# Performance work log

Measured on AMD Instinct MI355X. Metric: run time of the kernel, lower is better.

The kernel has to match this reference:

```python
import jax, jax.numpy as jnp
import numpy as np

B, S, D, NH, DH = 2, 1024, 1024, 16, 64
BLOCK_SIZES = [4, 4, 4]
SCALE = 1.0 / (DH ** 0.5)
INF = 1000000.0
LN_EPS = 1e-9


def _pos_embeds(seq_len, d_model):
    # Funnel 'factorized' sinusoidal relative position embeddings (phi, pi, psi, omega)
    pos = jnp.arange(seq_len, dtype=jnp.float32)
    freq = jnp.arange(d_model // 2, dtype=jnp.float32)
    inv_freq = 1.0 / (10000.0 ** (freq / (d_model // 2)))
    sinusoid = pos[:, None] * inv_freq[None]
    s, c = jnp.sin(sinusoid), jnp.cos(sinusoid)
    phi = jnp.concatenate([s, s], axis=-1)
    psi = jnp.concatenate([c, s], axis=-1)
    pi = jnp.concatenate([c, c], axis=-1)
    omega = jnp.concatenate([-s, c], axis=-1)
    return phi, pi, psi, omega


def _layer_norm(x, g, b):
    mu = jnp.mean(x, axis=-1, keepdims=True)
    var = jnp.mean((x - mu) ** 2, axis=-1, keepdims=True)
    return (x - mu) * jax.lax.rsqrt(var + LN_EPS) * g + b


def _attn_layer(q_in, kv, phi_q, pi_q, psi_k, om_k, tt_mat, mask, W):
    # FunnelRelMultiheadAttentionDecoder.forward (dropout=0, eval)
    (wq, bq, wk, bk, wv, bv, rw, rr, rs, rk, seg, wp, bp, g, b) = W
    Bq, Lq, _ = q_in.shape
    Lk = kv.shape[1]
    q = (q_in @ wq + bq).reshape(Bq, Lq, NH, DH) * SCALE
    k = (kv @ wk + bk).reshape(Bq, Lk, NH, DH)
    v = (kv @ wv + bv).reshape(Bq, Lk, NH, DH)
    content = jnp.einsum('bind,bjnd->bnij', q + rw * SCALE, k)
    # factorized relative positional attention
    q_r = jnp.einsum('binh,dnh->bind', q + rr * SCALE, rk)  # [B,Lq,NH,D]
    pos = (jnp.einsum('bind,jd->bnij', q_r * phi_q[:, None], psi_k)
           + jnp.einsum('bind,jd->bnij', q_r * pi_q[:, None], om_k))
    # relative token-type attention
    ttb = jnp.einsum('bind,snd->bnis', q + rs * SCALE, seg)  # [B,NH,Lq,2]
    tok = jnp.where(tt_mat[:, None], ttb[..., 1:2], ttb[..., 0:1])
    score = (content + pos + tok).astype(jnp.float32)
    score = score - INF * (1.0 - mask[:, None, :, None].astype(jnp.float32))
    prob = jax.nn.softmax(score, axis=-1).astype(q_in.dtype)
    vec = jnp.einsum('bnij,bjnd->bind', prob, v).reshape(Bq, Lq, NH * DH)
    return _layer_norm(q_in + vec @ wp + bp, g, b)


def _upsample(h, target):
    # _upsample_hidden: interleave hidden with avg of (hidden, roll(hidden, 1))
    shifted = jnp.roll(h, 1, axis=1)
    interp = 0.5 * (h + shifted)
    out = jnp.stack([h, interp], axis=2).reshape(h.shape[0], -1, h.shape[2])
    if out.shape[1] > target:
        out = out[:, :-1]
    return out


def _forward(final_hidden, block_h0, block_h1, block_h2, attention_mask, token_type_ids,
             Wq, bq, Wk, bk, Wv, bv, r_w_bias, r_r_bias, r_s_bias, r_kernel, seg_embed,
             Wpost, bpost, ln_g, ln_b):
    block_hs = [block_h0, block_h1, block_h2]
    # init_attention_inputs
    ids = token_type_ids
    cls_ids = ids == 2
    tt = (ids[:, :, None] == ids[:, None]) | (cls_ids[:, :, None] | cls_ids[:, None])
    phi, pi, psi, omega = _pos_embeds(S, D)
    mask = attention_mask
    # replay encoder-side pooling schedule (pool_q_only, separate_cls=False)
    inputs = {}
    for bi, bs in enumerate(BLOCK_SIZES):
        pooling = bi > 0
        if pooling:
            phi, pi = phi[::2], pi[::2]          # pre_attention_pooling
            tt = tt[:, ::2, :]
        for li in range(bs):
            inputs[(bi, li)] = (phi, pi, psi, omega, tt, mask)
            if li == 0 and pooling:              # post_attention_pooling
                psi, omega = psi[::2], omega[::2]
                tt = tt[:, :, ::2]
                mask = jnp.min(mask.reshape(mask.shape[0], -1, 2), axis=-1)
    # decoder pass (skip_w == 0 so skip mixing is identity)
    offsets = np.cumsum([0] + BLOCK_SIZES)
    hidden = final_hidden
    for bi in reversed(range(len(BLOCK_SIZES))):
        upflag = hidden.shape[1] < block_hs[0].shape[1] and bi > 0
        if upflag:
            up = _upsample(hidden, block_hs[bi - 1].shape[1])
        for li in reversed(range(BLOCK_SIZES[bi])):
            l = int(offsets[bi]) + li
            phi_, pi_, psi_, om_, tt_, m_ = inputs[(bi, li)]
            do_up = upflag and li == 0
            if do_up:
                q_in, kv = up, hidden
                # query is the long (pre-pool) side: use context-length phi/pi on keys
                phi_q, pi_q, psi_k, om_k = psi_, om_, phi_, pi_
            else:
                q_in = kv = hidden
                phi_q, pi_q, psi_k, om_k = phi_, pi_, psi_, om_
            W = (Wq[l], bq[l], Wk[l], bk[l], Wv[l], bv[l], r_w_bias[l], r_r_bias[l],
                 r_s_bias[l], r_kernel[l], seg_embed[l], Wpost[l], bpost[l], ln_g[l], ln_b[l])
            hidden = _attn_layer(q_in, kv, phi_q, pi_q, psi_k, om_k,
                                 jnp.swapaxes(tt_, 1, 2), m_, W)
    return hidden


def setup_inputs() -> dict:
    key = jax.random.key(0)
    ks = jax.random.split(key, 20)
    L = sum(BLOCK_SIZES)
    w = lambda k, shape: jax.random.normal(k, shape, dtype=jnp.float32) * 0.02
    return {
        'final_hidden': jax.random.normal(ks[0], (B, S // 4, D), dtype=jnp.float32),
        'block_h0': jax.random.normal(ks[1], (B, S, D), dtype=jnp.float32),
        'block_h1': jax.random.normal(ks[2], (B, S // 2, D), dtype=jnp.float32),
        'block_h2': jax.random.normal(ks[3], (B, S // 4, D), dtype=jnp.float32),
        'attention_mask': jnp.ones((B, S), dtype=jnp.float32),
        'token_type_ids': jax.random.randint(ks[4], (B, S), 0, 2, dtype=jnp.int32),
        'Wq': w(ks[5], (L, D, D)), 'bq': jnp.zeros((L, D), jnp.float32),
        'Wk': w(ks[6], (L, D, D)), 'bk': jnp.zeros((L, D), jnp.float32),
        'Wv': w(ks[7], (L, D, D)), 'bv': jnp.zeros((L, D), jnp.float32),
        'r_w_bias': w(ks[8], (L, NH, DH)),
        'r_r_bias': w(ks[9], (L, NH, DH)),
        'r_s_bias': w(ks[10], (L, NH, DH)),
        'r_kernel': w(ks[11], (L, D, NH, DH)),
        'seg_embed': w(ks[12], (L, 2, NH, DH)),
        'Wpost': w(ks[13], (L, D, D)), 'bpost': jnp.zeros((L, D), jnp.float32),
        'ln_g': jnp.ones((L, D), jnp.float32), 'ln_b': jnp.zeros((L, D), jnp.float32),
    }


def reference(final_hidden, block_h0, block_h1, block_h2, attention_mask, token_type_ids,
              Wq, bq, Wk, bk, Wv, bv, r_w_bias, r_r_bias, r_s_bias, r_kernel, seg_embed,
              Wpost, bpost, ln_g, ln_b):
    return _forward(final_hidden, block_h0, block_h1, block_h2, attention_mask,
                    token_type_ids, Wq, bq, Wk, bk, Wv, bv, r_w_bias, r_r_bias,
                    r_s_bias, r_kernel, seg_embed, Wpost, bpost, ln_g, ln_b)
```

## Files before the change

kernel.cpp:

```cpp
#include <hip/hip_runtime.h>
#include <math.h>

#define NHEAD 16
#define DMODEL 1024
#define BATCH 2
#define QSCALE 0.125f

typedef __attribute__((ext_vector_type(8))) short bf16x8;
typedef __attribute__((ext_vector_type(4))) float f32x4;

__device__ inline unsigned short f2bf(float x) {
  unsigned int u = __float_as_uint(x);
  u += 0x7FFF + ((u >> 16) & 1);
  return (unsigned short)(u >> 16);
}
__device__ inline float bf2f(unsigned short h) {
  return __uint_as_float(((unsigned int)h) << 16);
}

typedef __attribute__((address_space(1))) const unsigned int gu32;
typedef __attribute__((address_space(3))) unsigned int lu32;
__device__ inline void gl_lds16(const unsigned short* g, unsigned short* l) {
  __builtin_amdgcn_global_load_lds((gu32*)g, (lu32*)l, 16, 0, 0);
}

template<int MODE>
__global__ __launch_bounds__(256) void gemm_bf16(
    const unsigned short* __restrict__ A, const unsigned short* __restrict__ Bt,
    const float* __restrict__ bias, const unsigned short* __restrict__ R,
    void* __restrict__ Cv, int M, int N, int K, int nrel)
{
  __shared__ __align__(16) unsigned short smem[32 * 512];
  const int tid = threadIdx.x;
  const int lane = tid & 63, w = tid >> 6;
  const int mw = w >> 1, nw = w & 1;
  const int bm = blockIdx.x * 128, bn = blockIdx.y * 128;
  const int lm = lane & 15, lq = lane >> 4;
  float* Cf = (float*)Cv;
  unsigned short* Cb = (unsigned short*)Cv;

  f32x4 acc[4][4];
#pragma unroll
  for (int i = 0; i < 4; ++i)
#pragma unroll
    for (int j = 0; j < 4; ++j) acc[i][j] = (f32x4){0.f, 0.f, 0.f, 0.f};

  for (int k0 = 0; k0 < K; k0 += 64) {
#pragma unroll
    for (int f = w; f < 16; f += 4) {
      const int kb = f >> 3, mb = f & 7;
      const int gr = bm + mb * 16 + lm;
      const int gc = k0 + kb * 32 + lq * 8;
      gl_lds16(A + (size_t)gr * K + gc, &smem[f * 512]);
      gl_lds16(Bt + (size_t)(bn + mb * 16 + lm) * K + gc, &smem[(16 + f) * 512]);
    }
    __syncthreads();
#pragma unroll
    for (int kb = 0; kb < 2; ++kb) {
      bf16x8 af[4], bf[4];
#pragma unroll
      for (int i = 0; i < 4; ++i)
        af[i] = *(const bf16x8*)(&smem[(kb * 8 + mw * 4 + i) * 512 + lane * 8]);
#pragma unroll
      for (int j = 0; j < 4; ++j)
        bf[j] = *(const bf16x8*)(&smem[(16 + kb * 8 + nw * 4 + j) * 512 + lane * 8]);
#pragma unroll
      for (int i = 0; i < 4; ++i)
#pragma unroll
        for (int j = 0; j < 4; ++j)
          acc[i][j] = __builtin_amdgcn_mfma_f32_16x16x32_bf16(
              af[i], bf[j], acc[i][j], 0, 0, 0);
    }
    __syncthreads();
  }
#pragma unroll
  for (int i = 0; i < 4; ++i) {
#pragma unroll
    for (int j = 0; j < 4; ++j) {
      const int col = bn + nw * 64 + j * 16 + lm;
      if (col >= N) continue;
#pragma unroll
      for (int r = 0; r < 4; ++r) {
        const int row = bm + mw * 64 + i * 16 + lq * 4 + r;
        float vv = acc[i][j][r];
        if (MODE == 1) vv = (vv + bias[col]) * QSCALE;
        else if (MODE == 2) vv = vv + bias[col] + bf2f(R[(size_t)row * N + col]);
        if (MODE == 3)
          Cb[(((size_t)(row >> 6)) * nrel + col) * 64 + (row & 63)] = f2bf(vv);
        else
          Cf[(size_t)row * N + col] = vv;
      }
    }
  }
}

__global__ __launch_bounds__(256) void gemm_qkv(
    const unsigned short* __restrict__ A, const unsigned short* __restrict__ Bt,
    const float* __restrict__ bq, const float* __restrict__ bk,
    const float* __restrict__ bv, float* __restrict__ Cq,
    unsigned short* __restrict__ Ck, unsigned short* __restrict__ Cv,
    int M, int K, int colbase)
{
  __shared__ __align__(16) unsigned short smem[32 * 512];
  const int tid = threadIdx.x;
  const int lane = tid & 63, w = tid >> 6;
  const int mw = w >> 1, nw = w & 1;
  const int bm = blockIdx.x * 128, bn = colbase + blockIdx.y * 128;
  const int lm = lane & 15, lq = lane >> 4;

  f32x4 acc[4][4];
#pragma unroll
  for (int i = 0; i < 4; ++i)
#pragma unroll
    for (int j = 0; j < 4; ++j) acc[i][j] = (f32x4){0.f, 0.f, 0.f, 0.f};

  for (int k0 = 0; k0 < K; k0 += 64) {
#pragma unroll
    for (int f = w; f < 16; f += 4) {
      const int kb = f >> 3, mb = f & 7;
      const int gr = bm + mb * 16 + lm;
      const int gc = k0 + kb * 32 + lq * 8;
      gl_lds16(A + (size_t)gr * K + gc, &smem[f * 512]);
      gl_lds16(Bt + (size_t)(bn + mb * 16 + lm) * K + gc, &smem[(16 + f) * 512]);
    }
    __syncthreads();
#pragma unroll
    for (int kb = 0; kb < 2; ++kb) {
      bf16x8 af[4], bf[4];
#pragma unroll
      for (int i = 0; i < 4; ++i)
        af[i] = *(const bf16x8*)(&smem[(kb * 8 + mw * 4 + i) * 512 + lane * 8]);
#pragma unroll
      for (int j = 0; j < 4; ++j)
        bf[j] = *(const bf16x8*)(&smem[(16 + kb * 8 + nw * 4 + j) * 512 + lane * 8]);
#pragma unroll
      for (int i = 0; i < 4; ++i)
#pragma unroll
        for (int j = 0; j < 4; ++j)
          acc[i][j] = __builtin_amdgcn_mfma_f32_16x16x32_bf16(
              af[i], bf[j], acc[i][j], 0, 0, 0);
    }
    __syncthreads();
  }
  const int which = bn >> 10;
  const float* bias = (which == 0) ? bq : (which == 1) ? bk : bv;
#pragma unroll
  for (int i = 0; i < 4; ++i) {
#pragma unroll
    for (int j = 0; j < 4; ++j) {
      const int col = bn + nw * 64 + j * 16 + lm;
      const int nc = col & 1023;
#pragma unroll
      for (int r = 0; r < 4; ++r) {
        const int row = bm + mw * 64 + i * 16 + lq * 4 + r;
        const float vv = acc[i][j][r] + bias[nc];
        if (which == 0)
          Cq[(size_t)row * 1024 + nc] = vv * QSCALE;
        else if (which == 1)
          Ck[(size_t)row * 1024 + nc] = f2bf(vv);
        else
          Cv[(size_t)row * 1024 + nc] = f2bf(vv);
      }
    }
  }
}

__global__ __launch_bounds__(256) void tpose5_k(
    const float* __restrict__ s0, const float* __restrict__ s1,
    const float* __restrict__ s2, const float* __restrict__ s3,
    const float* __restrict__ s4, unsigned short* __restrict__ d0,
    unsigned short* __restrict__ d1, unsigned short* __restrict__ d2,
    unsigned short* __restrict__ d3, unsigned short* __restrict__ d4)
{
  const float* in;
  unsigned short* out;
  switch (blockIdx.z) {
    case 0: in = s0; out = d0; break;
    case 1: in = s1; out = d1; break;
    case 2: in = s2; out = d2; break;
    case 3: in = s3; out = d3; break;
    default: in = s4; out = d4; break;
  }
  __shared__ float t[32][33];
  const int bi = blockIdx.x * 32, bj = blockIdx.y * 32;
  const int r = threadIdx.x >> 3, c4 = (threadIdx.x & 7) * 4;
  const float4 v = *(const float4*)(in + (size_t)(bi + r) * 1024 + bj + c4);
  t[r][c4] = v.x; t[r][c4 + 1] = v.y; t[r][c4 + 2] = v.z; t[r][c4 + 3] = v.w;
  __syncthreads();
  ushort4 o;
  o.x = f2bf(t[c4 + 0][r]); o.y = f2bf(t[c4 + 1][r]);
  o.z = f2bf(t[c4 + 2][r]); o.w = f2bf(t[c4 + 3][r]);
  *(ushort4*)(out + (size_t)(bj + r) * 1024 + bi + c4) = o;
}

__global__ void cvt_k(const float* __restrict__ in,
                      unsigned short* __restrict__ out, int n)
{
  const int i = blockIdx.x * 256 + threadIdx.x;
  if (i < n) out[i] = f2bf(in[i]);
}

__global__ void trig_fill(unsigned short* __restrict__ T, int rPad, int rmin,
                          int rstep, float sgn)
{
  const int idx = blockIdx.x * 256 + threadIdx.x;
  if (idx >= rPad * 512) return;
  const int r = idx >> 9, f = idx & 511;
  const float invf = expf((float)f * -(9.210340371976184f / 512.0f));
  const float ang = (float)(rmin + r * rstep) * invf;
  float s, c;
  sincosf(ang, &s, &c);
  T[(size_t)r * 1024 + f] = f2bf(sgn * s);
  T[(size_t)r * 1024 + f + 512] = f2bf(c);
}

__global__ void upsample_k(const unsigned short* __restrict__ h,
                           unsigned short* __restrict__ out, int L)
{
  const size_t idx = (size_t)blockIdx.x * 256 + threadIdx.x;
  const size_t total = (size_t)BATCH * 2 * L * DMODEL;
  if (idx >= total) return;
  const int d = (int)(idx & 1023);
  const int t2 = (int)((idx >> 10) % (size_t)(2 * L));
  const int b = (int)((idx >> 10) / (size_t)(2 * L));
  const unsigned short* hb = h + (size_t)b * L * DMODEL;
  float val;
  if ((t2 & 1) == 0) {
    val = bf2f(hb[(size_t)(t2 >> 1) * DMODEL + d]);
  } else {
    const int t = (t2 - 1) >> 1;
    const int prev = (t == 0) ? (L - 1) : (t - 1);
    val = 0.5f * (bf2f(hb[(size_t)t * DMODEL + d]) +
                  bf2f(hb[(size_t)prev * DMODEL + d]));
  }
  out[idx] = f2bf(val);
}

template<bool BF16OUT>
__global__ __launch_bounds__(256) void ln_k(
    const float* __restrict__ x, const float* __restrict__ g,
    const float* __restrict__ b, void* __restrict__ outv)
{
  const int row = blockIdx.x;
  const int tid = threadIdx.x;
  const float* xr = x + (size_t)row * DMODEL;
  const float4 xv = *(const float4*)(xr + tid * 4);
  __shared__ float red[4];
  float s = xv.x + xv.y + xv.z + xv.w;
#pragma unroll
  for (int off = 32; off > 0; off >>= 1) s += __shfl_down(s, off, 64);
  if ((tid & 63) == 0) red[tid >> 6] = s;
  __syncthreads();
  const float mean = (red[0] + red[1] + red[2] + red[3]) * (1.f / 1024.f);
  const float dx = xv.x - mean, dy = xv.y - mean;
  const float dz = xv.z - mean, dw = xv.w - mean;
  float vs = dx * dx + dy * dy + dz * dz + dw * dw;
  __syncthreads();
#pragma unroll
  for (int off = 32; off > 0; off >>= 1) vs += __shfl_down(vs, off, 64);
  if ((tid & 63) == 0) red[tid >> 6] = vs;
  __syncthreads();
  const float var = (red[0] + red[1] + red[2] + red[3]) * (1.f / 1024.f);
  const float rstd = rsqrtf(var + 1e-9f);
  const float4 gv = *(const float4*)(g + tid * 4);
  const float4 bv = *(const float4*)(b + tid * 4);
  const float ox = dx * rstd * gv.x + bv.x;
  const float oy = dy * rstd * gv.y + bv.y;
  const float oz = dz * rstd * gv.z + bv.z;
  const float ow = dw * rstd * gv.w + bv.w;
  if (BF16OUT) {
    ushort4 o = {f2bf(ox), f2bf(oy), f2bf(oz), f2bf(ow)};
    *(ushort4*)((unsigned short*)outv + (size_t)row * DMODEL + tid * 4) = o;
  } else {
    float4 o = {ox, oy, oz, ow};
    *(float4*)((float*)outv + (size_t)row * DMODEL + tid * 4) = o;
  }
}

template<int TK>
__global__ __launch_bounds__(256) void attn_mfma(
    const float* __restrict__ q, const unsigned short* __restrict__ k,
    const unsigned short* __restrict__ v, const unsigned short* __restrict__ wrel,
    const float* __restrict__ rw, const float* __restrict__ rr,
    const float* __restrict__ rs, const float* __restrict__ seg,
    const int* __restrict__ ids, unsigned short* __restrict__ vec,
    int Lq, int Lk, int sq, int sk, int sqp, int skp, int rbase, int nrel)
{
  constexpr int NTJ = TK / 16;
  constexpr int NKF = TK / 8;
  constexpr int VSTR = TK + 8;
  constexpr int PFS = 132;
  __shared__ __align__(16) unsigned short kF[NKF * 512];
  __shared__ __align__(16) unsigned short bandF[16 * 512];
  __shared__ __align__(16) unsigned short vT[64 * VSTR];
  __shared__ __align__(16) unsigned short PSm[64 * VSTR];
  __shared__ float pfS[64 * PFS];
  __shared__ float tb0S[64], tb1S[64];
  __shared__ int idqS[64], idkS[TK];

  const int tid = threadIdx.x;
  const int lane = tid & 63, w = tid >> 6;
  const int lm = lane & 15, lq = lane >> 4;
  const int b = blockIdx.z, n = blockIdx.y;
  const int i0 = blockIdx.x * 64;

  bf16x8 qwf[2], q2f[2];
  {
    const float* qrow = q + ((size_t)b * Lq + i0 + w * 16 + lm) * DMODEL + n * 64;
    const float* rwp = rw + n * 64;
    const float* rrp = rr + n * 64;
#pragma unroll
    for (int ks = 0; ks < 2; ++ks) {
      const int c0 = ks * 32 + lq * 8;
      float qv[8], wv[8], rv[8];
      *(float4*)&qv[0] = *(const float4*)(qrow + c0);
      *(float4*)&qv[4] = *(const float4*)(qrow + c0 + 4);
      *(float4*)&wv[0] = *(const float4*)(rwp + c0);
      *(float4*)&wv[4] = *(const float4*)(rwp + c0 + 4);
      *(float4*)&rv[0] = *(const float4*)(rrp + c0);
      *(float4*)&rv[4] = *(const float4*)(rrp + c0 + 4);
#pragma unroll
      for (int e = 0; e < 8; ++e) {
        qwf[ks][e] = (short)f2bf(qv[e] + wv[e] * QSCALE);
        q2f[ks][e] = (short)f2bf(qv[e] + rv[e] * QSCALE);
      }
    }
  }
  if (tid < 128) {
    const int i = tid >> 1, s_ = tid & 1;
    const float* qr = q + ((size_t)b * Lq + i0 + i) * DMODEL + n * 64;
    const float* sg = seg + (s_ * NHEAD + n) * 64;
    const float* rsp = rs + n * 64;
    float a = 0.f;
    for (int h = 0; h < 64; ++h) a += (qr[h] + rsp[h] * QSCALE) * sg[h];
    if (s_) tb1S[i] = a; else tb0S[i] = a;
  }
  if (tid < 64) idqS[tid] = ids[b * 1024 + sq * (i0 + tid)];

  f32x4 oacc[4];
#pragma unroll
  for (int th = 0; th < 4; ++th) oacc[th] = (f32x4){0.f, 0.f, 0.f, 0.f};
  float mrun[4], lrun[4];
#pragma unroll
  for (int rg = 0; rg < 4; ++rg) { mrun[rg] = -1e30f; lrun[rg] = 0.f; }

  const int W = sqp * 63 + skp * (TK - 1) + 1;
  const int ibase = w * 16 + lq * 4;

  for (int jt = 0; jt < Lk; jt += TK) {
    __syncthreads();
    {
      const unsigned short* kb = k + ((size_t)b * Lk + jt) * DMODEL + n * 64;
#pragma unroll
      for (int f = w; f < NKF; f += 4) {
        const int tj = f >> 1, ks = f & 1;
        gl_lds16(kb + (size_t)(tj * 16 + lm) * DMODEL + ks * 32 + lq * 8,
                 &kF[f * 512]);
      }
    }
    const int rlo = sqp * i0 - skp * (jt + TK - 1) + rbase;
    {
      const unsigned short* wb = wrel + ((size_t)n * nrel + rlo) * 64;
#pragma unroll
      for (int f = w; f < 16; f += 4) {
        const int rt = f >> 1, ks = f & 1;
        const int r = rt * 16 + lm;
        const int rc = r < W ? r : W - 1;
        gl_lds16(wb + (size_t)rc * 64 + ks * 32 + lq * 8, &bandF[f * 512]);
      }
    }
    {
      const unsigned short* vb = v + ((size_t)b * Lk + jt) * DMODEL + n * 64;
      if (TK == 64) {
        const int j2 = tid & 31, h0 = (tid >> 5) * 8;
        const uint4 a0 = *(const uint4*)(vb + (size_t)(2 * j2) * DMODEL + h0);
        const uint4 a1 = *(const uint4*)(vb + (size_t)(2 * j2 + 1) * DMODEL + h0);
        const unsigned short* p0 = (const unsigned short*)&a0;
        const unsigned short* p1 = (const unsigned short*)&a1;
#pragma unroll
        for (int e = 0; e < 8; ++e)
          *(unsigned int*)&vT[(h0 + e) * VSTR + 2 * j2] =
              (unsigned int)p0[e] | ((unsigned int)p1[e] << 16);
      } else {
        if (tid < 128) {
          const int j2 = tid & 15, h0 = ((tid >> 4) & 7) * 8;
          const uint4 a0 = *(const uint4*)(vb + (size_t)(2 * j2) * DMODEL + h0);
          const uint4 a1 = *(const uint4*)(vb + (size_t)(2 * j2 + 1) * DMODEL + h0);
          const unsigned short* p0 = (const unsigned short*)&a0;
          const unsigned short* p1 = (const unsigned short*)&a1;
#pragma unroll
          for (int e = 0; e < 8; ++e)
            *(unsigned int*)&vT[(h0 + e) * VSTR + 2 * j2] =
                (unsigned int)p0[e] | ((unsigned int)p1[e] << 16);
        }
      }
    }
    if (tid < TK) idkS[tid] = ids[b * 1024 + sk * (jt + tid)];
    __syncthreads();

    f32x4 cacc[NTJ];
#pragma unroll
    for (int tj = 0; tj < NTJ; ++tj) cacc[tj] = (f32x4){0.f, 0.f, 0.f, 0.f};
    f32x4 pacc[8];
#pragma unroll
    for (int rt = 0; rt < 8; ++rt) pacc[rt] = (f32x4){0.f, 0.f, 0.f, 0.f};
    __builtin_amdgcn_s_setprio(1);
#pragma unroll
    for (int ks = 0; ks < 2; ++ks) {
#pragma unroll
      for (int tj = 0; tj < NTJ; ++tj) {
        const bf16x8 kf = *(const bf16x8*)&kF[(tj * 2 + ks) * 512 + lane * 8];
        cacc[tj] = __builtin_amdgcn_mfma_f32_16x16x32_bf16(
            qwf[ks], kf, cacc[tj], 0, 0, 0);
      }
#pragma unroll
      for (int rt = 0; rt < 8; ++rt) {
        const bf16x8 bf_ = *(const bf16x8*)&bandF[(rt * 2 + ks) * 512 + lane * 8];
        pacc[rt] = __builtin_amdgcn_mfma_f32_16x16x32_bf16(
            q2f[ks], bf_, pacc[rt], 0, 0, 0);
      }
    }
    __builtin_amdgcn_s_setprio(0);
#pragma unroll
    for (int rt = 0; rt < 8; ++rt)
#pragma unroll
      for (int rg = 0; rg < 4; ++rg)
        pfS[(ibase + rg) * PFS + rt * 16 + lm] = pacc[rt][rg];

    float sreg[NTJ][4];
#pragma unroll
    for (int tj = 0; tj < NTJ; ++tj) {
      const int jl = tj * 16 + lm;
      const int ik = idkS[jl];
      const int rb_ = skp * (TK - 1 - jl);
#pragma unroll
      for (int rg = 0; rg < 4; ++rg) {
        const int iw = ibase + rg;
        const int ril = sqp * iw + rb_;
        const int iq = idqS[iw];
        const int sel = (iq == ik) | (iq == 2) | (ik == 2);
        sreg[tj][rg] = cacc[tj][rg] + pfS[iw * PFS + ril] +
                       (sel ? tb1S[iw] : tb0S[iw]);
      }
    }
#pragma unroll
    for (int rg = 0; rg < 4; ++rg) {
      float mx = sreg[0][rg];
#pragma unroll
      for (int tj = 1; tj < NTJ; ++tj) mx = fmaxf(mx, sreg[tj][rg]);
#pragma unroll
      for (int off = 1; off < 16; off <<= 1)
        mx = fmaxf(mx, __shfl_xor(mx, off, 64));
      const float mold = mrun[rg];
      const float mnew = fmaxf(mold, mx);
      float sum = 0.f;
#pragma unroll
      for (int tj = 0; tj < NTJ; ++tj) {
        const float p = __expf(sreg[tj][rg] - mnew);
        const unsigned short pb = f2bf(p);
        PSm[(ibase + rg) * VSTR + tj * 16 + lm] = pb;
        sum += bf2f(pb);
      }
#pragma unroll
      for (int off = 1; off < 16; off <<= 1) sum += __shfl_xor(sum, off, 64);
      const float al = __expf(mold - mnew);
      lrun[rg] = lrun[rg] * al + sum;
      mrun[rg] = mnew;
      oacc[0][rg] *= al; oacc[1][rg] *= al;
      oacc[2][rg] *= al; oacc[3][rg] *= al;
    }
    __builtin_amdgcn_s_setprio(1);
#pragma unroll
    for (int ks = 0; ks < TK / 32; ++ks) {
      const bf16x8 pa =
          *(const bf16x8*)&PSm[(w * 16 + lm) * VSTR + ks * 32 + lq * 8];
#pragma unroll
      for (int th = 0; th < 4; ++th) {
        const bf16x8 vf =
            *(const bf16x8*)&vT[(th * 16 + lm) * VSTR + ks * 32 + lq * 8];
        oacc[th] = __builtin_amdgcn_mfma_f32_16x16x32_bf16(
            pa, vf, oacc[th], 0, 0, 0);
      }
    }
    __builtin_amdgcn_s_setprio(0);
  }
  unsigned short* ob =
      vec + ((size_t)b * Lq + i0 + ibase) * DMODEL + n * 64 + lm;
#pragma unroll
  for (int rg = 0; rg < 4; ++rg) {
    const float linv = 1.f / lrun[rg];
#pragma unroll
    for (int th = 0; th < 4; ++th)
      ob[(size_t)rg * DMODEL + th * 16] = f2bf(oacc[th][rg] * linv);
  }
}

extern "C" void kernel_launch(void* const* d_in, const int* in_sizes, int n_in,
                              void* d_out, int out_size, void* d_ws,
                              size_t ws_size, hipStream_t stream)
{
  const float* final_hidden = (const float*)d_in[0];
  const int* ids = (const int*)d_in[5];
  const float* Wq = (const float*)d_in[6];
  const float* bq = (const float*)d_in[7];
  const float* Wk = (const float*)d_in[8];
  const float* bk = (const float*)d_in[9];
  const float* Wv = (const float*)d_in[10];
  const float* bvv = (const float*)d_in[11];
  const float* rw = (const float*)d_in[12];
  const float* rr = (const float*)d_in[13];
  const float* rs = (const float*)d_in[14];
  const float* rk = (const float*)d_in[15];
  const float* seg = (const float*)d_in[16];
  const float* Wp = (const float*)d_in[17];
  const float* bp = (const float*)d_in[18];
  const float* lng = (const float*)d_in[19];
  const float* lnb = (const float*)d_in[20];

  unsigned char* w8 = (unsigned char*)d_ws;
  const size_t MB = 1024 * 1024;
  unsigned short* hA    = (unsigned short*)(w8 + 0 * MB);
  unsigned short* hB    = (unsigned short*)(w8 + 4 * MB);
  unsigned short* upB   = (unsigned short*)(w8 + 8 * MB);
  float*          qB    = (float*)(w8 + 12 * MB);
  float*          pB    = (float*)(w8 + 20 * MB);
  unsigned short* kBf   = (unsigned short*)(w8 + 28 * MB);
  unsigned short* vBf   = (unsigned short*)(w8 + 32 * MB);
  unsigned short* vecB  = (unsigned short*)(w8 + 36 * MB);
  unsigned short* wrelB = (unsigned short*)(w8 + 40 * MB);
  unsigned short* wqkv  = (unsigned short*)(w8 + 45 * MB);
  unsigned short* wtp   = (unsigned short*)(w8 + 51 * MB);
  unsigned short* rkT   = (unsigned short*)(w8 + 53 * MB);
  unsigned short* trigA = (unsigned short*)(w8 + 55 * MB);

  {
    const int n = BATCH * 256 * DMODEL;
    cvt_k<<<dim3((n + 255) / 256), 256, 0, stream>>>(final_hidden, hA, n);
  }
  trig_fill<<<dim3((2048 * 512 + 255) / 256), 256, 0, stream>>>(
      trigA + (size_t)0 * 1024, 2048, -1023, 1, 1.f);
  trig_fill<<<dim3((2048 * 512 + 255) / 256), 256, 0, stream>>>(
      trigA + (size_t)2048 * 1024, 2048, -1022, 1, -1.f);
  trig_fill<<<dim3((1024 * 512 + 255) / 256), 256, 0, stream>>>(
      trigA + (size_t)4096 * 1024, 1024, -1022, 2, 1.f);
  trig_fill<<<dim3((1024 * 512 + 255) / 256), 256, 0, stream>>>(
      trigA + (size_t)5120 * 1024, 1024, -1020, 2, -1.f);
  trig_fill<<<dim3((512 * 512 + 255) / 256), 256, 0, stream>>>(
      trigA + (size_t)6144 * 1024, 512, -1020, 4, 1.f);

  const unsigned short* X = hA;

  for (int l = 11; l >= 0; --l) {
    int Lq, Lk, sq, sk, sqp, skp, nrel, rbase, troff;
    if (l <= 3)      { Lq=1024; Lk=1024; sq=1; sk=1; sqp=1; skp=1; nrel=2047; rbase=1023; troff=0; }
    else if (l == 4) { Lq=1024; Lk= 512; sq=1; sk=2; sqp=1; skp=2; nrel=2046; rbase=1022; troff=2048; }
    else if (l <= 7) { Lq= 512; Lk= 512; sq=2; sk=2; sqp=1; skp=1; nrel=1023; rbase= 511; troff=4096; }
    else if (l == 8) { Lq= 512; Lk= 256; sq=2; sk=4; sqp=1; skp=2; nrel=1022; rbase= 510; troff=5120; }
    else             { Lq= 256; Lk= 256; sq=4; sk=4; sqp=1; skp=1; nrel= 511; rbase= 255; troff=6144; }

    if (l == 11) {
      const size_t total = (size_t)BATCH * 512 * DMODEL;
      upsample_k<<<dim3((unsigned)((total + 255) / 256)), 256, 0, stream>>>(
          X, upB, 256);
    } else if (l == 7) {
      const size_t total = (size_t)BATCH * 1024 * DMODEL;
      upsample_k<<<dim3((unsigned)((total + 255) / 256)), 256, 0, stream>>>(
          X, upB, 512);
    }
    const bool doUp = (l == 8) || (l == 4);
    const unsigned short* Xq = doUp ? upB : X;
    const int Mq = BATCH * Lq, Mk = BATCH * Lk;
    const int rPad = ((nrel + 127) / 128) * 128;

    tpose5_k<<<dim3(32, 32, 5), 256, 0, stream>>>(
        Wq + (size_t)l * DMODEL * DMODEL, Wk + (size_t)l * DMODEL * DMODEL,
        Wv + (size_t)l * DMODEL * DMODEL, Wp + (size_t)l * DMODEL * DMODEL,
        rk + (size_t)l * DMODEL * DMODEL,
        wqkv, wqkv + (size_t)DMODEL * DMODEL, wqkv + (size_t)2 * DMODEL * DMODEL,
        wtp, rkT);

    gemm_bf16<3><<<dim3(DMODEL / 128, rPad / 128), 256, 0, stream>>>(
        rkT, trigA + (size_t)troff * 1024, nullptr, nullptr, wrelB,
        DMODEL, nrel, DMODEL, nrel);

    if (doUp) {
      gemm_bf16<1><<<dim3(Mq / 128, 8), 256, 0, stream>>>(
          Xq, wqkv, bq + l * DMODEL, nullptr, qB, Mq, DMODEL, DMODEL, 0);
      gemm_qkv<<<dim3(Mk / 128, 16), 256, 0, stream>>>(
          X, wqkv, bq + l * DMODEL, bk + l * DMODEL, bvv + l * DMODEL,
          qB, kBf, vBf, Mk, DMODEL, 1024);
    } else {
      gemm_qkv<<<dim3(Mq / 128, 24), 256, 0, stream>>>(
          X, wqkv, bq + l * DMODEL, bk + l * DMODEL, bvv + l * DMODEL,
          qB, kBf, vBf, Mq, DMODEL, 0);
    }

    dim3 ag(Lq / 64, NHEAD, BATCH);
    if (skp == 1)
      attn_mfma<64><<<ag, 256, 0, stream>>>(qB, kBf, vBf, wrelB,
          rw + l * NHEAD * 64, rr + l * NHEAD * 64, rs + l * NHEAD * 64,
          seg + l * 2 * NHEAD * 64, ids, vecB,
          Lq, Lk, sq, sk, sqp, skp, rbase, nrel);
    else
      attn_mfma<32><<<ag, 256, 0, stream>>>(qB, kBf, vBf, wrelB,
          rw + l * NHEAD * 64, rr + l * NHEAD * 64, rs + l * NHEAD * 64,
          seg + l * 2 * NHEAD * 64, ids, vecB,
          Lq, Lk, sq, sk, sqp, skp, rbase, nrel);

    gemm_bf16<2><<<dim3(Mq / 128, 8), 256, 0, stream>>>(
        vecB, wtp, bp + l * DMODEL, Xq, pB, Mq, DMODEL, DMODEL, 0);
    if (l == 0) {
      ln_k<false><<<dim3(Mq), 256, 0, stream>>>(
          pB, lng + l * DMODEL, lnb + l * DMODEL, d_out);
    } else {
      unsigned short* outBuf = (X == hA) ? hB : hA;
      ln_k<true><<<dim3(Mq), 256, 0, stream>>>(
          pB, lng + l * DMODEL, lnb + l * DMODEL, outBuf);
      X = outBuf;
    }
  }
  (void)in_sizes; (void)n_in; (void)out_size; (void)ws_size;
}
```

Before: 2.134 ms.

## Double-buffer attention K/band/V tiles and trim relative-position band MFMAs per wave

Moves the attention kernel's K, relative-band and V tile loads into a two-stage ping-pong buffer, so the next tile's global loads are issued while the current tile is computed. Each wave now computes only the 5 band row-tiles it actually needs instead of all 8. The per-wave score and probability scratch reuses the staging buffer to save LDS. The change adds an extra barrier per iteration, holds V in registers across the loop, and hardcodes sqp=1 in the band index math, which is a correctness risk if sqp differs.

```diff
diff --git a/kernel.cpp b/kernel.cpp
--- a/kernel.cpp
+++ b/kernel.cpp
@@ -289,12 +289,11 @@
   constexpr int NTJ = TK / 16;
   constexpr int NKF = TK / 8;
   constexpr int VSTR = TK + 8;
-  constexpr int PFS = 132;
-  __shared__ __align__(16) unsigned short kF[NKF * 512];
-  __shared__ __align__(16) unsigned short bandF[16 * 512];
-  __shared__ __align__(16) unsigned short vT[64 * VSTR];
-  __shared__ __align__(16) unsigned short PSm[64 * VSTR];
-  __shared__ float pfS[64 * PFS];
+  constexpr int SB_STAGE = (NKF + 16) * 1024;
+  constexpr int WREG = 5504;
+  constexpr int SB = (SB_STAGE > 4 * WREG) ? SB_STAGE : 4 * WREG;
+  __shared__ __align__(16) unsigned char Sb[2][SB];
+  __shared__ __align__(16) unsigned short vT[2][64 * VSTR];
   __shared__ float tb0S[64], tb1S[64];
   __shared__ int idqS[64], idkS[TK];
 
@@ -303,6 +302,9 @@
   const int lm = lane & 15, lq = lane >> 4;
   const int b = blockIdx.z, n = blockIdx.y;
   const int i0 = blockIdx.x * 64;
+  const int W = 64 + skp * (TK - 1);
+  const int ibase = w * 16 + lq * 4;
+  const int nt = Lk / TK;
 
   bf16x8 qwf[2], q2f[2];
   {
@@ -337,6 +339,11 @@
   }
   if (tid < 64) idqS[tid] = ids[b * 1024 + sq * (i0 + tid)];
 
+  int vj2, vh0;
+  if (TK == 64) { vj2 = tid & 31; vh0 = (tid >> 5) * 8; }
+  else          { vj2 = tid & 15; vh0 = ((tid >> 4) & 7) * 8; }
+  const bool vact = (TK == 64) || (tid < 128);
+
   f32x4 oacc[4];
 #pragma unroll
   for (int th = 0; th < 4; ++th) oacc[th] = (f32x4){0.f, 0.f, 0.f, 0.f};
@@ -344,66 +351,80 @@
 #pragma unroll
   for (int rg = 0; rg < 4; ++rg) { mrun[rg] = -1e30f; lrun[rg] = 0.f; }
 
-  const int W = sqp * 63 + skp * (TK - 1) + 1;
-  const int ibase = w * 16 + lq * 4;
-
-  for (int jt = 0; jt < Lk; jt += TK) {
+  auto STAGE = [&](int jt, int bufi) {
+    unsigned short* kF = (unsigned short*)&Sb[bufi][0];
+    unsigned short* bF = (unsigned short*)&Sb[bufi][NKF * 1024];
+    const unsigned short* kb = k + ((size_t)b * Lk + jt) * DMODEL + n * 64;
+#pragma unroll
+    for (int f = w; f < NKF; f += 4) {
+      const int tj = f >> 1, ks = f & 1;
+      gl_lds16(kb + (size_t)(tj * 16 + lm) * DMODEL + ks * 32 + lq * 8,
+               &kF[f * 512]);
+    }
+    const int rlo = i0 - skp * (jt + TK - 1) + rbase;
+    const unsigned short* wb = wrel + ((size_t)n * nrel + rlo) * 64;
+#pragma unroll
+    for (int f = w; f < 16; f += 4) {
+      const int rt = f >> 1, ks = f & 1;
+      const int r = rt * 16 + lm;
+      const int rc = r < W ? r : W - 1;
+      gl_lds16(wb + (size_t)rc * 64 + ks * 32 + lq * 8, &bF[f * 512]);
+    }
+  };
+  uint4 vA0, vA1, vB0, vB1;
+  auto VLOAD = [&](int jt, uint4& a0, uint4& a1) {
+    if (vact) {
+      const unsigned short* vb = v + ((size_t)b * Lk + jt) * DMODEL + n * 64;
+      a0 = *(const uint4*)(vb + (size_t)(2 * vj2) * DMODEL + vh0);
+      a1 = *(const uint4*)(vb + (size_t)(2 * vj2 + 1) * DMODEL + vh0);
+    }
+  };
+  auto VSTORE = [&](int bufi, const uint4& a0, const uint4& a1) {
+    if (vact) {
+      const unsigned short* p0 = (const unsigned short*)&a0;
+      const unsigned short* p1 = (const unsigned short*)&a1;
+      unsigned short* vt = &vT[bufi][0];
+#pragma unroll
+      for (int e = 0; e < 8; ++e)
+        *(unsigned int*)&vt[(vh0 + e) * VSTR + 2 * vj2] =
+            (unsigned int)p0[e] | ((unsigned int)p1[e] << 16);
+    }
+  };
+  int ridk = 0;
+
+  STAGE(0, 0);
+  VLOAD(0, vA0, vA1);
+  if (tid < TK) ridk = ids[b * 1024 + sk * tid];
+
+  for (int t = 0; t < nt; ++t) {
+    const int jt = t * TK;
+    const int buf = t & 1;
     __syncthreads();
-    {
-      const unsigned short* kb = k + ((size_t)b * Lk + jt) * DMODEL + n * 64;
-#pragma unroll
-      for (int f = w; f < NKF; f += 4) {
-        const int tj = f >> 1, ks = f & 1;
-        gl_lds16(kb + (size_t)(tj * 16 + lm) * DMODEL + ks * 32 + lq * 8,
-                 &kF[f * 512]);
-      }
-    }
-    const int rlo = sqp * i0 - skp * (jt + TK - 1) + rbase;
-    {
-      const unsigned short* wb = wrel + ((size_t)n * nrel + rlo) * 64;
-#pragma unroll
-      for (int f = w; f < 16; f += 4) {
-        const int rt = f >> 1, ks = f & 1;
-        const int r = rt * 16 + lm;
-        const int rc = r < W ? r : W - 1;
-        gl_lds16(wb + (size_t)rc * 64 + ks * 32 + lq * 8, &bandF[f * 512]);
-      }
-    }
-    {
-      const unsigned short* vb = v + ((size_t)b * Lk + jt) * DMODEL + n * 64;
-      if (TK == 64) {
-        const int j2 = tid & 31, h0 = (tid >> 5) * 8;
-        const uint4 a0 = *(const uint4*)(vb + (size_t)(2 * j2) * DMODEL + h0);
-        const uint4 a1 = *(const uint4*)(vb + (size_t)(2 * j2 + 1) * DMODEL + h0);
-        const unsigned short* p0 = (const unsigned short*)&a0;
-        const unsigned short* p1 = (const unsigned short*)&a1;
-#pragma unroll
-        for (int e = 0; e < 8; ++e)
-          *(unsigned int*)&vT[(h0 + e) * VSTR + 2 * j2] =
-              (unsigned int)p0[e] | ((unsigned int)p1[e] << 16);
-      } else {
-        if (tid < 128) {
-          const int j2 = tid & 15, h0 = ((tid >> 4) & 7) * 8;
-          const uint4 a0 = *(const uint4*)(vb + (size_t)(2 * j2) * DMODEL + h0);
-          const uint4 a1 = *(const uint4*)(vb + (size_t)(2 * j2 + 1) * DMODEL + h0);
-          const unsigned short* p0 = (const unsigned short*)&a0;
-          const unsigned short* p1 = (const unsigned short*)&a1;
-#pragma unroll
-          for (int e = 0; e < 8; ++e)
-            *(unsigned int*)&vT[(h0 + e) * VSTR + 2 * j2] =
-                (unsigned int)p0[e] | ((unsigned int)p1[e] << 16);
-        }
-      }
-    }
-    if (tid < TK) idkS[tid] = ids[b * 1024 + sk * (jt + tid)];
-    __syncthreads();
-
+    __builtin_amdgcn_sched_barrier(0);
+    if (tid < TK) idkS[tid] = ridk;
+    if (buf == 0) {
+      VSTORE(0, vA0, vA1);
+      if (t + 1 < nt) VLOAD(jt + TK, vB0, vB1);
+    } else {
+      VSTORE(1, vB0, vB1);
+      if (t + 1 < nt) VLOAD(jt + TK, vA0, vA1);
+    }
+    if (t + 1 < nt) {
+      STAGE(jt + TK, buf ^ 1);
+      if (tid < TK) ridk = ids[b * 1024 + sk * (jt + TK + tid)];
+    }
+    asm volatile("s_waitcnt lgkmcnt(0)" ::: "memory");
+    __builtin_amdgcn_s_barrier();
+    __builtin_amdgcn_sched_barrier(0);
+
+    const unsigned short* kF = (const unsigned short*)&Sb[buf][0];
+    const unsigned short* bF = (const unsigned short*)&Sb[buf][NKF * 1024];
     f32x4 cacc[NTJ];
 #pragma unroll
     for (int tj = 0; tj < NTJ; ++tj) cacc[tj] = (f32x4){0.f, 0.f, 0.f, 0.f};
-    f32x4 pacc[8];
-#pragma unroll
-    for (int rt = 0; rt < 8; ++rt) pacc[rt] = (f32x4){0.f, 0.f, 0.f, 0.f};
+    f32x4 pacc[5];
+#pragma unroll
+    for (int rt = 0; rt < 5; ++rt) pacc[rt] = (f32x4){0.f, 0.f, 0.f, 0.f};
     __builtin_amdgcn_s_setprio(1);
 #pragma unroll
     for (int ks = 0; ks < 2; ++ks) {
@@ -414,35 +435,41 @@
             qwf[ks], kf, cacc[tj], 0, 0, 0);
       }
 #pragma unroll
-      for (int rt = 0; rt < 8; ++rt) {
-        const bf16x8 bf_ = *(const bf16x8*)&bandF[(rt * 2 + ks) * 512 + lane * 8];
+      for (int rt = 0; rt < 5; ++rt) {
+        const bf16x8 bfr =
+            *(const bf16x8*)&bF[((w + rt) * 2 + ks) * 512 + lane * 8];
         pacc[rt] = __builtin_amdgcn_mfma_f32_16x16x32_bf16(
-            q2f[ks], bf_, pacc[rt], 0, 0, 0);
+            q2f[ks], bfr, pacc[rt], 0, 0, 0);
       }
     }
     __builtin_amdgcn_s_setprio(0);
-#pragma unroll
-    for (int rt = 0; rt < 8; ++rt)
+    asm volatile("s_waitcnt lgkmcnt(0)" ::: "memory");
+    __builtin_amdgcn_s_barrier();
+    __builtin_amdgcn_sched_barrier(0);
+
+    float* pfW = (float*)&Sb[buf][w * WREG];
+#pragma unroll
+    for (int rt = 0; rt < 5; ++rt)
 #pragma unroll
       for (int rg = 0; rg < 4; ++rg)
-        pfS[(ibase + rg) * PFS + rt * 16 + lm] = pacc[rt][rg];
+        pfW[(lq * 4 + rg) * 85 + rt * 16 + lm] = pacc[rt][rg];
 
     float sreg[NTJ][4];
 #pragma unroll
     for (int tj = 0; tj < NTJ; ++tj) {
       const int jl = tj * 16 + lm;
       const int ik = idkS[jl];
-      const int rb_ = skp * (TK - 1 - jl);
+      const int roff = skp * (TK - 1 - jl);
 #pragma unroll
       for (int rg = 0; rg < 4; ++rg) {
         const int iw = ibase + rg;
-        const int ril = sqp * iw + rb_;
         const int iq = idqS[iw];
         const int sel = (iq == ik) | (iq == 2) | (ik == 2);
-        sreg[tj][rg] = cacc[tj][rg] + pfS[iw * PFS + ril] +
+        sreg[tj][rg] = cacc[tj][rg] + pfW[(lq * 4 + rg) * 85 + lq * 4 + rg + roff] +
                        (sel ? tb1S[iw] : tb0S[iw]);
       }
     }
+    unsigned short* PSw = (unsigned short*)&Sb[buf][w * WREG];
 #pragma unroll
     for (int rg = 0; rg < 4; ++rg) {
       float mx = sreg[0][rg];
@@ -458,7 +485,7 @@
       for (int tj = 0; tj < NTJ; ++tj) {
         const float p = __expf(sreg[tj][rg] - mnew);
         const unsigned short pb = f2bf(p);
-        PSm[(ibase + rg) * VSTR + tj * 16 + lm] = pb;
+        PSw[(lq * 4 + rg) * VSTR + tj * 16 + lm] = pb;
         sum += bf2f(pb);
       }
 #pragma unroll
@@ -472,12 +499,11 @@
     __builtin_amdgcn_s_setprio(1);
 #pragma unroll
     for (int ks = 0; ks < TK / 32; ++ks) {
-      const bf16x8 pa =
-          *(const bf16x8*)&PSm[(w * 16 + lm) * VSTR + ks * 32 + lq * 8];
+      const bf16x8 pa = *(const bf16x8*)&PSw[lm * VSTR + ks * 32 + lq * 8];
 #pragma unroll
       for (int th = 0; th < 4; ++th) {
         const bf16x8 vf =
-            *(const bf16x8*)&vT[(th * 16 + lm) * VSTR + ks * 32 + lq * 8];
+            *(const bf16x8*)&vT[buf][(th * 16 + lm) * VSTR + ks * 32 + lq * 8];
         oacc[th] = __builtin_amdgcn_mfma_f32_16x16x32_bf16(
             pa, vf, oacc[th], 0, 0, 0);
       }
```

New measurement: 2.119 ms. About the same (-0.7%).
